# Kernel optimization log

Measured on AMD Instinct MI355X. Metric: run time of the kernel, lower is better.

Reference implementation:

```python
import jax, jax.numpy as jnp
import numpy as np
import math

N_NODES = 100000
N_EDGES = 1600000
IN_C, HID_C, OUT_C = 512, 128, 64
N_LAYERS = 8
ALPHA = 0.1
THETA = 0.5


def setup_inputs() -> dict:
    key = jax.random.key(0)
    ks = jax.random.split(key, 6)
    x = jax.random.normal(ks[0], (N_NODES, IN_C), dtype=jnp.float32)
    edge_index = jax.random.randint(ks[1], (2, N_EDGES), 0, N_NODES, dtype=jnp.int32)
    edge_weight = jax.random.uniform(ks[2], (N_EDGES,), dtype=jnp.float32)
    # parameters (scaled for numerical sanity)
    W_enc = jax.random.normal(ks[3], (HID_C, IN_C), dtype=jnp.float32) * (1.0 / math.sqrt(IN_C))
    W_convs = jax.random.normal(ks[4], (N_LAYERS, HID_C, HID_C), dtype=jnp.float32) * (1.0 / math.sqrt(HID_C))
    W_dec = jax.random.normal(ks[5], (OUT_C, HID_C), dtype=jnp.float32) * (1.0 / math.sqrt(HID_C))
    return {"x": x, "edge_index": edge_index, "edge_weight": edge_weight,
            "W_enc": W_enc, "W_convs": W_convs, "W_dec": W_dec}


def reference(x, edge_index, edge_weight, W_enc, W_convs, W_dec):
    # eval mode: dropout is a no-op
    src, dst = edge_index[0], edge_index[1]
    h = x @ W_enc.T                      # [N, HID]
    x0 = h                               # initial residual
    for i in range(N_LAYERS):
        # sparse neighbor aggregation: agg[d] = sum_e w_e * h[src_e]
        msg = h[src] * edge_weight[:, None]                      # [E, HID]
        agg = jax.ops.segment_sum(msg, dst, num_segments=N_NODES)
        hh = (1.0 - ALPHA) * agg + ALPHA * x0                    # initial residual
        beta = math.log(THETA / (i + 1) + 1.0)                   # identity mapping weight
        h = jax.nn.relu((1.0 - beta) * hh + beta * (hh @ W_convs[i]))
    return h @ W_dec.T                   # [N, OUT]
```

## Files before the change

### kernel.cpp

```cpp
#include <hip/hip_runtime.h>
#include <math.h>

#define N_NODES 100000
#define N_EDGES 1600000
#define IN_C 512
#define HID_C 128
#define OUT_C 64
#define N_LAYERS 8
#define BINSTRIDE 18432

typedef short bf16x8 __attribute__((ext_vector_type(8)));
typedef float f32x4 __attribute__((ext_vector_type(4)));

static __device__ __forceinline__ ushort f2bf(float f) {
  uint u = __float_as_uint(f);
  u = (u + 0x7FFFu + ((u >> 16) & 1u)) >> 16;
  return (ushort)u;
}
static __device__ __forceinline__ float bflo(uint u) { return __uint_as_float(u << 16); }
static __device__ __forceinline__ float bfhi(uint u) { return __uint_as_float(u & 0xffff0000u); }

__global__ __launch_bounds__(128) void init_bincur(int* __restrict__ bincur) {
  bincur[threadIdx.x] = threadIdx.x * BINSTRIDE;
}

__global__ __launch_bounds__(256) void bin_scatter(const int* __restrict__ src,
                                                   const int* __restrict__ dst,
                                                   const float* __restrict__ w,
                                                   int* __restrict__ bincur,
                                                   uint2* __restrict__ bb) {
  __shared__ uint2 ebuf[2048];
  __shared__ int hist[128];
  __shared__ int lstart[128];
  __shared__ int gbase[128];
  int tid = threadIdx.x;
  int base = blockIdx.x * 2048;
  int cnt = N_EDGES - base;
  if (cnt > 2048) cnt = 2048;
  if (tid < 128) hist[tid] = 0;
  __syncthreads();
  uint pay[8];
  int bn[8], rk[8], dfull[8];
#pragma unroll
  for (int i = 0; i < 8; i++) {
    int idx = tid + i * 256;
    if (idx < cnt) {
      int e = base + idx;
      int d = dst[e];
      uint fb = __float_as_uint(w[e]) + 0x8000u;
      pay[i] = ((fb >> 16) << 17) | (uint)src[e];
      dfull[i] = d;
      bn[i] = d >> 10;
      rk[i] = atomicAdd(&hist[bn[i]], 1);
    }
  }
  __syncthreads();
  if (tid == 0) {
    int acc = 0;
    for (int b = 0; b < 128; b++) { lstart[b] = acc; acc += hist[b]; }
  }
  __syncthreads();
  if (tid < 128 && hist[tid] > 0) gbase[tid] = atomicAdd(&bincur[tid], hist[tid]);
  __syncthreads();
#pragma unroll
  for (int i = 0; i < 8; i++) {
    int idx = tid + i * 256;
    if (idx < cnt) ebuf[lstart[bn[i]] + rk[i]] = make_uint2(pay[i], (uint)dfull[i]);
  }
  __syncthreads();
#pragma unroll
  for (int i = 0; i < 8; i++) {
    int j = tid + i * 256;
    if (j < cnt) {
      uint2 v = ebuf[j];
      int b = (int)(v.y >> 10);
      bb[gbase[b] + (j - lstart[b])] = v;
    }
  }
}

__global__ __launch_bounds__(256) void bin_count(const uint2* __restrict__ bb,
                                                 const int* __restrict__ bincur,
                                                 int* __restrict__ cnt) {
  __shared__ int lc[1024];
  int b = blockIdx.x;
  int tid = threadIdx.x;
  for (int i = tid; i < 1024; i += 256) lc[i] = 0;
  __syncthreads();
  int beg = b * BINSTRIDE, end = bincur[b];
  for (int j = beg + tid; j < end; j += 256)
    atomicAdd(&lc[bb[j].y & 1023u], 1);
  __syncthreads();
  int n0 = b << 10;
  for (int i = tid; i < 1024; i += 256)
    if (n0 + i < N_NODES) cnt[n0 + i] = lc[i];
}

__global__ __launch_bounds__(256) void scan_block(const int* __restrict__ in,
                                                  int* __restrict__ out,
                                                  int* __restrict__ bsum, int n) {
  __shared__ int tsum[256];
  int t = threadIdx.x;
  int base = blockIdx.x * 1024 + t * 4;
  int v0 = (base + 0 < n) ? in[base + 0] : 0;
  int v1 = (base + 1 < n) ? in[base + 1] : 0;
  int v2 = (base + 2 < n) ? in[base + 2] : 0;
  int v3 = (base + 3 < n) ? in[base + 3] : 0;
  int s = v0 + v1 + v2 + v3;
  tsum[t] = s;
  __syncthreads();
  for (int off = 1; off < 256; off <<= 1) {
    int x = (t >= off) ? tsum[t - off] : 0;
    __syncthreads();
    tsum[t] += x;
    __syncthreads();
  }
  int excl = tsum[t] - s;
  int i0 = excl + v0, i1 = i0 + v1, i2 = i1 + v2, i3 = i2 + v3;
  if (base + 0 < n) out[base + 0] = i0;
  if (base + 1 < n) out[base + 1] = i1;
  if (base + 2 < n) out[base + 2] = i2;
  if (base + 3 < n) out[base + 3] = i3;
  if (t == 255 && bsum) bsum[blockIdx.x] = tsum[255];
}

__global__ __launch_bounds__(256) void finalize_rows(const int* __restrict__ incl,
                                                     const int* __restrict__ auxi,
                                                     int* __restrict__ row, int n) {
  int i = blockIdx.x * 256 + threadIdx.x;
  if (i < n) {
    int g = i >> 10;
    int off = g ? auxi[g - 1] : 0;
    row[i + 1] = incl[i] + off;
    if (i == 0) row[0] = 0;
  }
}

__global__ __launch_bounds__(256) void bin_place(const uint2* __restrict__ bb,
                                                 const int* __restrict__ bincur,
                                                 const int* __restrict__ row,
                                                 uint* __restrict__ epk) {
  __shared__ int lcur[1024];
  int b = blockIdx.x;
  int n0 = b << 10;
  int tid = threadIdx.x;
  for (int i = tid; i < 1024; i += 256) {
    int d = n0 + i;
    lcur[i] = (d < N_NODES) ? row[d] : 0;
  }
  __syncthreads();
  int beg = b * BINSTRIDE, end = bincur[b];
  for (int j = beg + tid; j < end; j += 256) {
    uint2 v = bb[j];
    int p = atomicAdd(&lcur[v.y & 1023u], 1);
    epk[p] = v.x;
  }
}

__global__ __launch_bounds__(256) void cast_weights(const float* __restrict__ we,
                                                    const float* __restrict__ wc,
                                                    const float* __restrict__ wd,
                                                    ushort* __restrict__ web,
                                                    ushort* __restrict__ wcb,
                                                    ushort* __restrict__ wdb) {
  int i = blockIdx.x * 256 + threadIdx.x;
  if (i < 128 * 512) web[i] = f2bf(we[i]);
  if (i < 8 * 128 * 128) {
    int layer = i >> 14, rem = i & 16383, k = rem >> 7, j = rem & 127;
    wcb[(layer << 14) + (j << 7) + k] = f2bf(wc[i]);
  }
  if (i < 64 * 128) wdb[i] = f2bf(wd[i]);
}

__global__ __launch_bounds__(256) void enc_mfma(const float* __restrict__ x,
                                                const ushort* __restrict__ wb,
                                                ushort* __restrict__ h) {
  __shared__ ushort xs[64][136];
  __shared__ ushort ws[128][136];
  int tid = threadIdx.x;
  size_t row0 = (size_t)blockIdx.x * 64;
  int lane = tid & 63;
  int wv = tid >> 6;
  int m0 = (wv >> 1) * 32;
  int n0 = (wv & 1) * 64;
  int arow = m0 + (lane & 15);
  int akb = (lane >> 4) * 8;
  f32x4 acc[2][4] = {};
  for (int kc = 0; kc < 4; kc++) {
    int k0 = kc * 128;
    __syncthreads();
#pragma unroll
    for (int i = 0; i < 8; i++) {
      int u = tid + i * 256;
      int r = u >> 5, c4 = u & 31;
      uint2 p = make_uint2(0u, 0u);
      if (row0 + r < N_NODES) {
        float4 v = *(const float4*)(x + (row0 + r) * IN_C + k0 + c4 * 4);
        p.x = (uint)f2bf(v.x) | ((uint)f2bf(v.y) << 16);
        p.y = (uint)f2bf(v.z) | ((uint)f2bf(v.w) << 16);
      }
      *(uint2*)&xs[r][c4 * 4] = p;
    }
#pragma unroll
    for (int i = 0; i < 8; i++) {
      int u = tid + i * 256;
      int c = u >> 4, o = u & 15;
      *(uint4*)&ws[c][o * 8] = *(const uint4*)(wb + (size_t)c * IN_C + k0 + o * 8);
    }
    __syncthreads();
#pragma unroll
    for (int ks = 0; ks < 4; ks++) {
      int kk = ks * 32 + akb;
      bf16x8 a0 = *(bf16x8*)&xs[arow][kk];
      bf16x8 a1 = *(bf16x8*)&xs[arow + 16][kk];
#pragma unroll
      for (int n = 0; n < 4; n++) {
        bf16x8 b = *(bf16x8*)&ws[n0 + n * 16 + (lane & 15)][kk];
        acc[0][n] = __builtin_amdgcn_mfma_f32_16x16x32_bf16(a0, b, acc[0][n], 0, 0, 0);
        acc[1][n] = __builtin_amdgcn_mfma_f32_16x16x32_bf16(a1, b, acc[1][n], 0, 0, 0);
      }
    }
  }
  int crow = m0 + (lane >> 4) * 4;
  int ccol = lane & 15;
#pragma unroll
  for (int m = 0; m < 2; m++)
#pragma unroll
    for (int n = 0; n < 4; n++)
#pragma unroll
      for (int r = 0; r < 4; r++) {
        size_t rr = row0 + crow + m * 16 + r;
        if (rr < N_NODES)
          h[rr * HID_C + n0 + n * 16 + ccol] = f2bf(acc[m][n][r]);
      }
}

__global__ __launch_bounds__(256) void agg_bf(const ushort* __restrict__ h,
                                              const ushort* __restrict__ x0,
                                              const int* __restrict__ row,
                                              const uint* __restrict__ epk,
                                              ushort* __restrict__ out) {
  int node = (blockIdx.x * 256 + threadIdx.x) >> 6;
  int lane = threadIdx.x & 63;
  int beg = row[node], end = row[node + 1];
  float a0 = 0.f, a1 = 0.f;
  const uint* hp = (const uint*)h + lane;
  for (int e = beg; e < end; e += 16) {
    uint pv[16];
    uint hv[16];
#pragma unroll
    for (int k = 0; k < 16; k++) pv[k] = (e + k < end) ? epk[e + k] : 0u;
#pragma unroll
    for (int k = 0; k < 16; k++) hv[k] = hp[(size_t)(pv[k] & 0x1FFFFu) * 64];
#pragma unroll
    for (int k = 0; k < 16; k++) {
      float w = __uint_as_float((pv[k] >> 17) << 16);
      a0 = fmaf(w, bflo(hv[k]), a0);
      a1 = fmaf(w, bfhi(hv[k]), a1);
    }
  }
  uint xv = ((const uint*)x0)[(size_t)node * 64 + lane];
  float o0 = 0.9f * a0 + 0.1f * bflo(xv);
  float o1 = 0.9f * a1 + 0.1f * bfhi(xv);
  ((uint*)out)[(size_t)node * 64 + lane] = (uint)f2bf(o0) | ((uint)f2bf(o1) << 16);
}

__global__ __launch_bounds__(256) void conv_mfma(ushort* __restrict__ hbuf,
                                                 const ushort* __restrict__ wb,
                                                 float onemb, float beta) {
  __shared__ ushort hs[64][136];
  __shared__ ushort ws[128][136];
  int tid = threadIdx.x;
  size_t row0 = (size_t)blockIdx.x * 64;
#pragma unroll
  for (int i = 0; i < 4; i++) {
    int u = tid + i * 256;
    int r = u >> 4, o = u & 15;
    if (row0 + r < N_NODES)
      *(uint4*)&hs[r][o * 8] = *(const uint4*)(hbuf + (row0 + r) * HID_C + o * 8);
  }
#pragma unroll
  for (int i = 0; i < 8; i++) {
    int u = tid + i * 256;
    int c = u >> 4, o = u & 15;
    *(uint4*)&ws[c][o * 8] = *(const uint4*)(wb + (size_t)c * HID_C + o * 8);
  }
  __syncthreads();
  int lane = tid & 63;
  int wv = tid >> 6;
  int m0 = wv * 16;
  int arow = m0 + (lane & 15), akb = (lane >> 4) * 8;
  f32x4 acc[8] = {};
#pragma unroll
  for (int ks = 0; ks < 4; ks++) {
    int kk = ks * 32 + akb;
    bf16x8 a = *(bf16x8*)&hs[arow][kk];
#pragma unroll
    for (int n = 0; n < 8; n++) {
      bf16x8 b = *(bf16x8*)&ws[n * 16 + (lane & 15)][kk];
      acc[n] = __builtin_amdgcn_mfma_f32_16x16x32_bf16(a, b, acc[n], 0, 0, 0);
    }
  }
  int crow = m0 + (lane >> 4) * 4, ccol = lane & 15;
#pragma unroll
  for (int n = 0; n < 8; n++)
#pragma unroll
    for (int r = 0; r < 4; r++) {
      if (row0 + crow + r < N_NODES) {
        float hv = bflo((uint)hs[crow + r][n * 16 + ccol]);
        float o = fmaxf(onemb * hv + beta * acc[n][r], 0.f);
        hbuf[(row0 + crow + r) * HID_C + n * 16 + ccol] = f2bf(o);
      }
    }
}

__global__ __launch_bounds__(256) void dec_mfma(const ushort* __restrict__ h,
                                                const ushort* __restrict__ wb,
                                                float* __restrict__ out) {
  __shared__ ushort hs[32][136];
  __shared__ ushort ws[64][136];
  int tid = threadIdx.x;
  size_t row0 = (size_t)blockIdx.x * 32;
  {
    int r = tid >> 3, o = tid & 7;
    *(uint4*)&hs[r][o * 16] = *(const uint4*)(h + (row0 + r) * HID_C + o * 16);
    *(uint4*)&hs[r][o * 16 + 8] = *(const uint4*)(h + (row0 + r) * HID_C + o * 16 + 8);
  }
#pragma unroll
  for (int i = 0; i < 4; i++) {
    int u = tid + i * 256;
    int c = u >> 4, o = u & 15;
    *(uint4*)&ws[c][o * 8] = *(const uint4*)(wb + (size_t)c * HID_C + o * 8);
  }
  __syncthreads();
  int lane = tid & 63, wv = tid >> 6;
  int m0 = (wv >> 1) * 16, n0 = (wv & 1) * 32;
  int arow = m0 + (lane & 15), akb = (lane >> 4) * 8;
  f32x4 acc[2] = {};
#pragma unroll
  for (int ks = 0; ks < 4; ks++) {
    int kk = ks * 32 + akb;
    bf16x8 a = *(bf16x8*)&hs[arow][kk];
#pragma unroll
    for (int n = 0; n < 2; n++) {
      bf16x8 b = *(bf16x8*)&ws[n0 + n * 16 + (lane & 15)][kk];
      acc[n] = __builtin_amdgcn_mfma_f32_16x16x32_bf16(a, b, acc[n], 0, 0, 0);
    }
  }
  int crow = m0 + (lane >> 4) * 4, ccol = lane & 15;
#pragma unroll
  for (int n = 0; n < 2; n++)
#pragma unroll
    for (int r = 0; r < 4; r++)
      out[(row0 + crow + r) * OUT_C + n0 + n * 16 + ccol] = acc[n][r];
}

extern "C" void kernel_launch(void* const* d_in, const int* in_sizes, int n_in,
                              void* d_out, int out_size, void* d_ws, size_t ws_size,
                              hipStream_t stream) {
  const float* x = (const float*)d_in[0];
  const int* ei = (const int*)d_in[1];
  const float* ew = (const float*)d_in[2];
  const float* Wenc = (const float*)d_in[3];
  const float* Wconvs = (const float*)d_in[4];
  const float* Wdec = (const float*)d_in[5];
  float* out = (float*)d_out;

  char* p = (char*)d_ws;
  ushort* H0 = (ushort*)p; p += (size_t)N_NODES * HID_C * 2;
  ushort* HA = (ushort*)p; p += (size_t)N_NODES * HID_C * 2;
  ushort* HB = (ushort*)p; p += (size_t)N_NODES * HID_C * 2;
  uint* EPK = (uint*)p;    p += (size_t)N_EDGES * 4;
  uint2* BB = (uint2*)p;   p += (size_t)128 * BINSTRIDE * 8;
  ushort* WENC = (ushort*)p;  p += 128 * 512 * 2;
  ushort* WCONV = (ushort*)p; p += 8 * 128 * 128 * 2;
  ushort* WDEC = (ushort*)p;  p += 64 * 128 * 2;
  int* ROW = (int*)p;  p += (N_NODES + 1) * 4;
  int* CNT = (int*)p;  p += N_NODES * 4;
  int* INCL = (int*)p; p += N_NODES * 4;
  int* BINCUR = (int*)p; p += 128 * 4;
  int* AUX = (int*)p;  p += 128 * 4;
  int* AUXI = (int*)p;

  const int* src = ei;
  const int* dst = ei + N_EDGES;

  cast_weights<<<512, 256, 0, stream>>>(Wenc, Wconvs, Wdec, WENC, WCONV, WDEC);

  init_bincur<<<1, 128, 0, stream>>>(BINCUR);
  bin_scatter<<<(N_EDGES + 2047) / 2048, 256, 0, stream>>>(src, dst, ew, BINCUR, BB);
  bin_count<<<98, 256, 0, stream>>>(BB, BINCUR, CNT);
  scan_block<<<98, 256, 0, stream>>>(CNT, INCL, AUX, N_NODES);
  scan_block<<<1, 256, 0, stream>>>(AUX, AUXI, nullptr, 98);
  finalize_rows<<<391, 256, 0, stream>>>(INCL, AUXI, ROW, N_NODES);
  bin_place<<<98, 256, 0, stream>>>(BB, BINCUR, ROW, EPK);

  enc_mfma<<<1563, 256, 0, stream>>>(x, WENC, H0);

  const ushort* cur = H0;
  ushort* bufs[2] = {HA, HB};
  for (int i = 0; i < N_LAYERS; i++) {
    ushort* nxt = bufs[i & 1];
    agg_bf<<<25000, 256, 0, stream>>>(cur, H0, ROW, EPK, nxt);
    float beta = logf(0.5f / (float)(i + 1) + 1.0f);
    conv_mfma<<<1563, 256, 0, stream>>>(nxt, WCONV + (size_t)i * HID_C * HID_C,
                                        1.0f - beta, beta);
    cur = nxt;
  }

  dec_mfma<<<3125, 256, 0, stream>>>(cur, WDEC, out);
}
```

Before: 820.1 us.

## Fuse CSR count, scan and placement into one per-bin kernel; shrink gather batch

```diff
diff --git a/kernel.cpp b/kernel.cpp
--- a/kernel.cpp
+++ b/kernel.cpp
@@ -7,6 +7,7 @@
 #define HID_C 128
 #define OUT_C 64
 #define N_LAYERS 8
+#define N_BINS 98
 #define BINSTRIDE 18432
 
 typedef short bf16x8 __attribute__((ext_vector_type(8)));
@@ -79,80 +80,56 @@
   }
 }
 
-__global__ __launch_bounds__(256) void bin_count(const uint2* __restrict__ bb,
-                                                 const int* __restrict__ bincur,
-                                                 int* __restrict__ cnt) {
+__global__ __launch_bounds__(64) void bin_base(const int* __restrict__ bincur,
+                                               int* __restrict__ base) {
+  if (threadIdx.x == 0) {
+    int acc = 0;
+    for (int b = 0; b < N_BINS; b++) {
+      base[b] = acc;
+      acc += bincur[b] - b * BINSTRIDE;
+    }
+  }
+}
+
+__global__ __launch_bounds__(256) void bin_finalize(const uint2* __restrict__ bb,
+                                                    const int* __restrict__ bincur,
+                                                    const int* __restrict__ base,
+                                                    int* __restrict__ row,
+                                                    uint* __restrict__ epk) {
   __shared__ int lc[1024];
-  int b = blockIdx.x;
-  int tid = threadIdx.x;
+  __shared__ int tsum[256];
+  int b = blockIdx.x, tid = threadIdx.x;
+  int n0 = b << 10;
   for (int i = tid; i < 1024; i += 256) lc[i] = 0;
   __syncthreads();
   int beg = b * BINSTRIDE, end = bincur[b];
   for (int j = beg + tid; j < end; j += 256)
     atomicAdd(&lc[bb[j].y & 1023u], 1);
   __syncthreads();
-  int n0 = b << 10;
-  for (int i = tid; i < 1024; i += 256)
-    if (n0 + i < N_NODES) cnt[n0 + i] = lc[i];
-}
-
-__global__ __launch_bounds__(256) void scan_block(const int* __restrict__ in,
-                                                  int* __restrict__ out,
-                                                  int* __restrict__ bsum, int n) {
-  __shared__ int tsum[256];
-  int t = threadIdx.x;
-  int base = blockIdx.x * 1024 + t * 4;
-  int v0 = (base + 0 < n) ? in[base + 0] : 0;
-  int v1 = (base + 1 < n) ? in[base + 1] : 0;
-  int v2 = (base + 2 < n) ? in[base + 2] : 0;
-  int v3 = (base + 3 < n) ? in[base + 3] : 0;
+  int i0 = tid * 4;
+  int v0 = lc[i0], v1 = lc[i0 + 1], v2 = lc[i0 + 2], v3 = lc[i0 + 3];
   int s = v0 + v1 + v2 + v3;
-  tsum[t] = s;
+  tsum[tid] = s;
   __syncthreads();
   for (int off = 1; off < 256; off <<= 1) {
-    int x = (t >= off) ? tsum[t - off] : 0;
+    int xx = (tid >= off) ? tsum[tid - off] : 0;
     __syncthreads();
-    tsum[t] += x;
+    tsum[tid] += xx;
     __syncthreads();
   }
-  int excl = tsum[t] - s;
-  int i0 = excl + v0, i1 = i0 + v1, i2 = i1 + v2, i3 = i2 + v3;
-  if (base + 0 < n) out[base + 0] = i0;
-  if (base + 1 < n) out[base + 1] = i1;
-  if (base + 2 < n) out[base + 2] = i2;
-  if (base + 3 < n) out[base + 3] = i3;
-  if (t == 255 && bsum) bsum[blockIdx.x] = tsum[255];
-}
-
-__global__ __launch_bounds__(256) void finalize_rows(const int* __restrict__ incl,
-                                                     const int* __restrict__ auxi,
-                                                     int* __restrict__ row, int n) {
-  int i = blockIdx.x * 256 + threadIdx.x;
-  if (i < n) {
-    int g = i >> 10;
-    int off = g ? auxi[g - 1] : 0;
-    row[i + 1] = incl[i] + off;
-    if (i == 0) row[0] = 0;
-  }
-}
-
-__global__ __launch_bounds__(256) void bin_place(const uint2* __restrict__ bb,
-                                                 const int* __restrict__ bincur,
-                                                 const int* __restrict__ row,
-                                                 uint* __restrict__ epk) {
-  __shared__ int lcur[1024];
-  int b = blockIdx.x;
-  int n0 = b << 10;
-  int tid = threadIdx.x;
-  for (int i = tid; i < 1024; i += 256) {
-    int d = n0 + i;
-    lcur[i] = (d < N_NODES) ? row[d] : 0;
-  }
-  __syncthreads();
-  int beg = b * BINSTRIDE, end = bincur[b];
+  int excl = tsum[tid] - s;
+  int gb = base[b];
+  int e0 = gb + excl, e1 = e0 + v0, e2 = e1 + v1, e3 = e2 + v2;
+  lc[i0] = e0; lc[i0 + 1] = e1; lc[i0 + 2] = e2; lc[i0 + 3] = e3;
+  if (n0 + i0 + 0 < N_NODES) row[n0 + i0 + 0] = e0;
+  if (n0 + i0 + 1 < N_NODES) row[n0 + i0 + 1] = e1;
+  if (n0 + i0 + 2 < N_NODES) row[n0 + i0 + 2] = e2;
+  if (n0 + i0 + 3 < N_NODES) row[n0 + i0 + 3] = e3;
+  if (b == ((N_NODES - 1) >> 10) && tid == 255) row[N_NODES] = gb + tsum[255];
+  __syncthreads();
   for (int j = beg + tid; j < end; j += 256) {
     uint2 v = bb[j];
-    int p = atomicAdd(&lcur[v.y & 1023u], 1);
+    int p = atomicAdd(&lc[v.y & 1023u], 1);
     epk[p] = v.x;
   }
 }
@@ -245,19 +222,39 @@
   int beg = row[node], end = row[node + 1];
   float a0 = 0.f, a1 = 0.f;
   const uint* hp = (const uint*)h + lane;
-  for (int e = beg; e < end; e += 16) {
-    uint pv[16];
-    uint hv[16];
-#pragma unroll
-    for (int k = 0; k < 16; k++) pv[k] = (e + k < end) ? epk[e + k] : 0u;
-#pragma unroll
-    for (int k = 0; k < 16; k++) hv[k] = hp[(size_t)(pv[k] & 0x1FFFFu) * 64];
-#pragma unroll
-    for (int k = 0; k < 16; k++) {
-      float w = __uint_as_float((pv[k] >> 17) << 16);
-      a0 = fmaf(w, bflo(hv[k]), a0);
-      a1 = fmaf(w, bfhi(hv[k]), a1);
-    }
+  for (int e = beg; e < end; e += 8) {
+    uint p0 = (e + 0 < end) ? epk[e + 0] : 0u;
+    uint p1 = (e + 1 < end) ? epk[e + 1] : 0u;
+    uint p2 = (e + 2 < end) ? epk[e + 2] : 0u;
+    uint p3 = (e + 3 < end) ? epk[e + 3] : 0u;
+    uint p4 = (e + 4 < end) ? epk[e + 4] : 0u;
+    uint p5 = (e + 5 < end) ? epk[e + 5] : 0u;
+    uint p6 = (e + 6 < end) ? epk[e + 6] : 0u;
+    uint p7 = (e + 7 < end) ? epk[e + 7] : 0u;
+    uint h0 = hp[(size_t)(p0 & 0x1FFFFu) * 64];
+    uint h1 = hp[(size_t)(p1 & 0x1FFFFu) * 64];
+    uint h2 = hp[(size_t)(p2 & 0x1FFFFu) * 64];
+    uint h3 = hp[(size_t)(p3 & 0x1FFFFu) * 64];
+    uint h4 = hp[(size_t)(p4 & 0x1FFFFu) * 64];
+    uint h5 = hp[(size_t)(p5 & 0x1FFFFu) * 64];
+    uint h6 = hp[(size_t)(p6 & 0x1FFFFu) * 64];
+    uint h7 = hp[(size_t)(p7 & 0x1FFFFu) * 64];
+    float w0 = __uint_as_float((p0 >> 17) << 16);
+    float w1 = __uint_as_float((p1 >> 17) << 16);
+    float w2 = __uint_as_float((p2 >> 17) << 16);
+    float w3 = __uint_as_float((p3 >> 17) << 16);
+    float w4 = __uint_as_float((p4 >> 17) << 16);
+    float w5 = __uint_as_float((p5 >> 17) << 16);
+    float w6 = __uint_as_float((p6 >> 17) << 16);
+    float w7 = __uint_as_float((p7 >> 17) << 16);
+    a0 = fmaf(w0, bflo(h0), a0); a1 = fmaf(w0, bfhi(h0), a1);
+    a0 = fmaf(w1, bflo(h1), a0); a1 = fmaf(w1, bfhi(h1), a1);
+    a0 = fmaf(w2, bflo(h2), a0); a1 = fmaf(w2, bfhi(h2), a1);
+    a0 = fmaf(w3, bflo(h3), a0); a1 = fmaf(w3, bfhi(h3), a1);
+    a0 = fmaf(w4, bflo(h4), a0); a1 = fmaf(w4, bfhi(h4), a1);
+    a0 = fmaf(w5, bflo(h5), a0); a1 = fmaf(w5, bfhi(h5), a1);
+    a0 = fmaf(w6, bflo(h6), a0); a1 = fmaf(w6, bfhi(h6), a1);
+    a0 = fmaf(w7, bflo(h7), a0); a1 = fmaf(w7, bfhi(h7), a1);
   }
   uint xv = ((const uint*)x0)[(size_t)node * 64 + lane];
   float o0 = 0.9f * a0 + 0.1f * bflo(xv);
@@ -376,11 +373,8 @@
   ushort* WCONV = (ushort*)p; p += 8 * 128 * 128 * 2;
   ushort* WDEC = (ushort*)p;  p += 64 * 128 * 2;
   int* ROW = (int*)p;  p += (N_NODES + 1) * 4;
-  int* CNT = (int*)p;  p += N_NODES * 4;
-  int* INCL = (int*)p; p += N_NODES * 4;
   int* BINCUR = (int*)p; p += 128 * 4;
-  int* AUX = (int*)p;  p += 128 * 4;
-  int* AUXI = (int*)p;
+  int* BASE = (int*)p;   p += 128 * 4;
 
   const int* src = ei;
   const int* dst = ei + N_EDGES;
@@ -389,11 +383,8 @@
 
   init_bincur<<<1, 128, 0, stream>>>(BINCUR);
   bin_scatter<<<(N_EDGES + 2047) / 2048, 256, 0, stream>>>(src, dst, ew, BINCUR, BB);
-  bin_count<<<98, 256, 0, stream>>>(BB, BINCUR, CNT);
-  scan_block<<<98, 256, 0, stream>>>(CNT, INCL, AUX, N_NODES);
-  scan_block<<<1, 256, 0, stream>>>(AUX, AUXI, nullptr, 98);
-  finalize_rows<<<391, 256, 0, stream>>>(INCL, AUXI, ROW, N_NODES);
-  bin_place<<<98, 256, 0, stream>>>(BB, BINCUR, ROW, EPK);
+  bin_base<<<1, 64, 0, stream>>>(BINCUR, BASE);
+  bin_finalize<<<N_BINS, 256, 0, stream>>>(BB, BINCUR, BASE, ROW, EPK);
 
   enc_mfma<<<1563, 256, 0, stream>>>(x, WENC, H0);
 
```

Result: no change. 804.3 us (-1.9%).
